# Kernel optimization log

Measured on AMD Instinct MI355X. Metric: run time of the kernel, lower is better.

Reference implementation:

```python
import jax, jax.numpy as jnp
import numpy as np

DIM = 2048
DIM_SEQ = 2048
HEADS = 4
BATCH = 4
LN_EPS = 1e-5  # torch nn.LayerNorm default


def setup_inputs() -> dict:
    key = jax.random.key(0)
    k1, k2 = jax.random.split(key)
    init_eps = 0.001 / DIM_SEQ
    x = jax.random.normal(k1, (BATCH, DIM_SEQ, DIM), dtype=jnp.float32)
    weight = jax.random.uniform(k2, (HEADS, DIM_SEQ, DIM_SEQ), dtype=jnp.float32,
                                minval=-init_eps, maxval=init_eps)
    bias = jnp.ones((HEADS, DIM_SEQ), dtype=jnp.float32)
    ln_gamma = jnp.ones((DIM // 2,), dtype=jnp.float32)
    ln_beta = jnp.zeros((DIM // 2,), dtype=jnp.float32)
    return {"x": x, "weight": weight, "bias": bias,
            "ln_gamma": ln_gamma, "ln_beta": ln_beta}


def _layernorm(x, gamma, beta):
    mu = jnp.mean(x, axis=-1, keepdims=True)
    var = jnp.mean(jnp.square(x - mu), axis=-1, keepdims=True)
    return (x - mu) * jax.lax.rsqrt(var + LN_EPS) * gamma + beta


def reference(x, weight, bias, ln_gamma, ln_beta):
    b, n, _ = x.shape
    h = HEADS
    res, gate = jnp.split(x, 2, axis=-1)          # each [b, n, dim/2]
    gate = _layernorm(gate, ln_gamma, ln_beta)
    w = weight[:, :n, :n]                          # [h, n, n]
    bi = bias[:, :n]                               # [h, n]
    # causal: zero strictly-upper triangle (output pos m attends n <= m)
    w = w * jnp.tril(jnp.ones((n, n), dtype=w.dtype))
    d = gate.shape[-1] // h
    gate = gate.reshape(b, n, h, d).transpose(0, 2, 1, 3)   # [b, h, n, d]
    gate = jnp.einsum('bhnd,hmn->bhmd', gate, w)
    gate = gate + bi[None, :, :, None]
    gate = gate.transpose(0, 2, 1, 3).reshape(b, n, h * d)  # [b, n, dim/2]
    return gate * res
```

## Files before the change

kernel.cpp:

```cpp
#include <hip/hip_runtime.h>
#include <hip/hip_bf16.h>

constexpr int Bb = 4;
constexpr int Nn = 2048;
constexpr int DX = 2048;
constexpr int GD = 1024;
constexpr int DH = 256;
constexpr int BM = 128, BD = 128, BK = 32;

typedef short short8v __attribute__((ext_vector_type(8)));
typedef short short4v __attribute__((ext_vector_type(4)));
typedef float f32x4   __attribute__((ext_vector_type(4)));

static __device__ __forceinline__ short f2bf(float f) {
    return __builtin_bit_cast(short, __float2bfloat16(f));
}

__global__ __launch_bounds__(256) void ln_stats_kernel(const float* __restrict__ x,
                                                       float2* __restrict__ mr) {
    int t = threadIdx.x;
    int row = blockIdx.x * 4 + (t >> 6);
    int lane = t & 63;
    const float4* xr = reinterpret_cast<const float4*>(x + (size_t)row * DX + GD);
    float s = 0.f, ss = 0.f;
#pragma unroll
    for (int q = 0; q < 4; ++q) {
        float4 v = xr[q * 64 + lane];
        s  += v.x + v.y + v.z + v.w;
        ss += v.x*v.x + v.y*v.y + v.z*v.z + v.w*v.w;
    }
#pragma unroll
    for (int off = 32; off >= 1; off >>= 1) {
        s  += __shfl_down(s,  off, 64);
        ss += __shfl_down(ss, off, 64);
    }
    if (lane == 0) {
        float m   = s * (1.f / GD);
        float var = ss * (1.f / GD) - m * m;
        mr[row] = make_float2(m, rsqrtf(var + 1e-5f));
    }
}

__global__ __launch_bounds__(256, 3) void sgu_mfma_kernel(
    const float* __restrict__ x, const float* __restrict__ w,
    const float* __restrict__ bias, const float* __restrict__ gamma,
    const float* __restrict__ beta, const float2* __restrict__ mr,
    float* __restrict__ out)
{
    __shared__ __align__(16) short Ws[2][BM * BK];
    __shared__ __align__(16) short Gs[2][BD * BK];
    __shared__ __align__(16) float2 MR[Nn];

    const int t  = threadIdx.x;
    const int bx = blockIdx.x;
    const int dc = bx & 1;
    const int h  = (bx >> 1) & 3;
    const int b  = bx >> 3;
    const int y  = blockIdx.y;
    const int mt = (y < 8) ? (15 - 2 * y) : ((y - 8) * 2);
    const int m0 = mt * BM;
    const int cb = h * DH + dc * BD;
    const int nk = 4 * mt + 4;

    const int lane = t & 63;
    const int wv = t >> 6;
    const int wm = wv >> 1, wc = wv & 1;
    const int g  = lane >> 4;
    const int lr = lane & 15;

    const int sw_row = t >> 1;
    const int sw_kh  = t & 1;
    const int sg_c4  = (t & 31) * 4;
    const int sg_k4  = (t >> 5) * 4;

    const float* xb   = x + (size_t)b * Nn * DX;
    const float* wrow = w + ((size_t)h * Nn + m0 + sw_row) * Nn + sw_kh * 16;
    const float* gsrc = xb + GD + cb + sg_c4;
    const float2* mrb = mr + b * Nn;

    float4 gmv = *reinterpret_cast<const float4*>(gamma + cb + sg_c4);
    float4 btv = *reinterpret_cast<const float4*>(beta  + cb + sg_c4);
    const float gmc[4] = {gmv.x, gmv.y, gmv.z, gmv.w};
    const float btc[4] = {btv.x, btv.y, btv.z, btv.w};

    f32x4 acc[4][4] = {};
    float4 wreg[4];
    float4 greg[4];

    auto LOADT = [&](int kt) {
        const int n0 = kt * BK;
#pragma unroll
        for (int q = 0; q < 4; ++q)
            wreg[q] = *reinterpret_cast<const float4*>(wrow + n0 + q * 4);
#pragma unroll
        for (int j = 0; j < 4; ++j)
            greg[j] = *reinterpret_cast<const float4*>(gsrc + (size_t)(n0 + sg_k4 + j) * DX);
    };

    auto STAGE = [&](int buf, int kt) {
        const int n0 = kt * BK;
        const int m = m0 + sw_row;
        short8v wlo, whi;
#pragma unroll
        for (int q = 0; q < 4; ++q) {
            float vv[4] = {wreg[q].x, wreg[q].y, wreg[q].z, wreg[q].w};
#pragma unroll
            for (int e = 0; e < 4; ++e) {
                int i = q * 4 + e;
                int n = n0 + sw_kh * 16 + i;
                short bfv = f2bf((n <= m) ? vv[e] : 0.f);
                if (i < 8) wlo[i] = bfv; else whi[i - 8] = bfv;
            }
        }
        char* wl = (char*)&Ws[buf][0];
        unsigned wb = (unsigned)(sw_row * 64 + sw_kh * 32);
        unsigned sz = ((unsigned)(sw_row >> 1) & 3u) << 4;
        *reinterpret_cast<short8v*>(wl + ((wb)      ^ sz)) = wlo;
        *reinterpret_cast<short8v*>(wl + ((wb + 16) ^ sz)) = whi;
        float muk[4], rsk[4];
        {
            f32x4 p0 = *reinterpret_cast<const f32x4*>(&MR[n0 + sg_k4]);
            f32x4 p1 = *reinterpret_cast<const f32x4*>(&MR[n0 + sg_k4 + 2]);
            muk[0] = p0[0]; rsk[0] = p0[1]; muk[1] = p0[2]; rsk[1] = p0[3];
            muk[2] = p1[0]; rsk[2] = p1[1]; muk[3] = p1[2]; rsk[3] = p1[3];
        }
        float gv[4][4];
        gv[0][0]=greg[0].x; gv[0][1]=greg[0].y; gv[0][2]=greg[0].z; gv[0][3]=greg[0].w;
        gv[1][0]=greg[1].x; gv[1][1]=greg[1].y; gv[1][2]=greg[1].z; gv[1][3]=greg[1].w;
        gv[2][0]=greg[2].x; gv[2][1]=greg[2].y; gv[2][2]=greg[2].z; gv[2][3]=greg[2].w;
        gv[3][0]=greg[3].x; gv[3][1]=greg[3].y; gv[3][2]=greg[3].z; gv[3][3]=greg[3].w;
        char* glp = (char*)&Gs[buf][0];
#pragma unroll
        for (int cc = 0; cc < 4; ++cc) {
            short4v pk;
#pragma unroll
            for (int j = 0; j < 4; ++j)
                pk[j] = f2bf((gv[j][cc] - muk[j]) * rsk[j] * gmc[cc] + btc[cc]);
            int c = sg_c4 + cc;
            unsigned off = (unsigned)(c * 64 + sg_k4 * 2);
            off ^= ((unsigned)(c >> 1) & 3u) << 4;
            *reinterpret_cast<short4v*>(glp + off) = pk;
        }
    };

    auto COMPUTE = [&](int buf) {
        const char* wl  = (const char*)&Ws[buf][0];
        const char* glp = (const char*)&Gs[buf][0];
        short8v af[4], bfr[4];
#pragma unroll
        for (int fi = 0; fi < 4; ++fi) {
            int row = wm * 64 + fi * 16 + lr;
            unsigned off = (unsigned)(row * 64 + g * 16);
            off ^= ((unsigned)(row >> 1) & 3u) << 4;
            af[fi] = *reinterpret_cast<const short8v*>(wl + off);
        }
#pragma unroll
        for (int fj = 0; fj < 4; ++fj) {
            int c = wc * 64 + fj * 16 + lr;
            unsigned off = (unsigned)(c * 64 + g * 16);
            off ^= ((unsigned)(c >> 1) & 3u) << 4;
            bfr[fj] = *reinterpret_cast<const short8v*>(glp + off);
        }
#pragma unroll
        for (int fi = 0; fi < 4; ++fi)
#pragma unroll
            for (int fj = 0; fj < 4; ++fj)
                acc[fi][fj] = __builtin_amdgcn_mfma_f32_16x16x32_bf16(
                    af[fi], bfr[fj], acc[fi][fj], 0, 0, 0);
    };

    const int nstage = nk * BK;
    for (int i = t; i < nstage; i += 256)
        MR[i] = mrb[i];
    LOADT(0);
    __syncthreads();
    STAGE(0, 0);
    __syncthreads();

    int cur = 0;
    for (int kt = 0; kt < nk; ++kt) {
        const bool more = (kt + 1 < nk);
        if (more) LOADT(kt + 1);
        COMPUTE(cur);
        if (more) STAGE(cur ^ 1, kt + 1);
        __syncthreads();
        cur ^= 1;
    }

#pragma unroll
    for (int fi = 0; fi < 4; ++fi) {
#pragma unroll
        for (int r = 0; r < 4; ++r) {
            int m = m0 + wm * 64 + fi * 16 + g * 4 + r;
            float bv = bias[h * Nn + m];
            const float* resrow = xb + (size_t)m * DX + cb;
            float* orow = out + ((size_t)b * Nn + m) * GD + cb;
#pragma unroll
            for (int fj = 0; fj < 4; ++fj) {
                int c = wc * 64 + fj * 16 + lr;
                orow[c] = (acc[fi][fj][r] + bv) * resrow[c];
            }
        }
    }
}

extern "C" void kernel_launch(void* const* d_in, const int* in_sizes, int n_in,
                              void* d_out, int out_size, void* d_ws, size_t ws_size,
                              hipStream_t stream) {
    const float* x     = (const float*)d_in[0];
    const float* w     = (const float*)d_in[1];
    const float* bias  = (const float*)d_in[2];
    const float* gamma = (const float*)d_in[3];
    const float* beta  = (const float*)d_in[4];
    float* out  = (float*)d_out;
    float2* mrw = (float2*)d_ws;

    ln_stats_kernel<<<Bb * Nn / 4, 256, 0, stream>>>(x, mrw);

    dim3 grid(32, 16, 1);
    sgu_mfma_kernel<<<grid, 256, 0, stream>>>(x, w, bias, gamma, beta, mrw, out);
}
```

Baseline: 253.2 us.

## Pre-convert weights and normalized gate to swizzled bf16 tiles, stage via direct LDS loads

Adds two pre-pass kernels. One converts the causal-masked weight to bf16 and the other applies layernorm to the gate and converts it to bf16. Both write tiles already in the swizzled LDS layout into workspace. The main GEMM kernel then fills shared memory with global_load_lds 16-byte copies instead of loading fp32 into registers and converting in the loop. This halves the bytes the main loop reads, moves conversion and normalization out of it, and frees registers. The cost is extra launches and an extra write and read of the bf16 copies, and the kernel returns without doing anything if the workspace is too small.

```diff
diff --git a/kernel.cpp b/kernel.cpp
--- a/kernel.cpp
+++ b/kernel.cpp
@@ -1,19 +1,24 @@
 #include <hip/hip_runtime.h>
 #include <hip/hip_bf16.h>
+
 
 constexpr int Bb = 4;
 constexpr int Nn = 2048;
 constexpr int DX = 2048;
 constexpr int GD = 1024;
 constexpr int DH = 256;
-constexpr int BM = 128, BD = 128, BK = 32;
 
 typedef short short8v __attribute__((ext_vector_type(8)));
-typedef short short4v __attribute__((ext_vector_type(4)));
 typedef float f32x4   __attribute__((ext_vector_type(4)));
 
 static __device__ __forceinline__ short f2bf(float f) {
     return __builtin_bit_cast(short, __float2bfloat16(f));
+}
+
+static __device__ __forceinline__ void gll16(const void* g, void* l) {
+    __builtin_amdgcn_global_load_lds(
+        (const __attribute__((address_space(1))) void*)g,
+        (__attribute__((address_space(3))) void*)l, 16, 0, 0);
 }
 
 __global__ __launch_bounds__(256) void ln_stats_kernel(const float* __restrict__ x,
@@ -41,15 +46,80 @@
     }
 }
 
+__global__ __launch_bounds__(256) void wcvt_kernel(const float* __restrict__ w,
+                                                   short* __restrict__ wt) {
+    const int hm = blockIdx.x;
+    const int kt = blockIdx.y;
+    const int mt = hm & 15, h = hm >> 4;
+    if (kt > 4 * mt + 3) return;
+    const int t = threadIdx.x;
+    const int m0 = mt * 128, n0 = kt * 32;
+    short* tile = wt + ((size_t)hm * 64 + kt) * 4096;
+#pragma unroll
+    for (int j = 0; j < 2; ++j) {
+        int s  = 2 * t + j;
+        int r  = s >> 2;
+        int k8 = (s & 3) ^ ((r >> 1) & 3);
+        const float* src = w + (size_t)(h * Nn + m0 + r) * Nn + n0 + k8 * 8;
+        float4 a = *reinterpret_cast<const float4*>(src);
+        float4 c = *reinterpret_cast<const float4*>(src + 4);
+        const int m = m0 + r, nb0 = n0 + k8 * 8;
+        float av[8] = {a.x, a.y, a.z, a.w, c.x, c.y, c.z, c.w};
+        short8v o;
+#pragma unroll
+        for (int e = 0; e < 8; ++e) o[e] = f2bf((nb0 + e) <= m ? av[e] : 0.f);
+        *reinterpret_cast<short8v*>(tile + s * 8) = o;
+    }
+}
+
+__global__ __launch_bounds__(256) void gcvt_kernel(const float* __restrict__ x,
+                                                   const float* __restrict__ gamma,
+                                                   const float* __restrict__ beta,
+                                                   const float2* __restrict__ mr,
+                                                   short* __restrict__ gt) {
+    __shared__ short T[128 * 136];
+    const int nb = blockIdx.x, cblk = blockIdx.y, b = blockIdx.z;
+    const int t = threadIdx.x;
+    const int n0b = nb * 128, c0 = cblk * 128;
+    const int c4 = (t & 31) * 4, rg = t >> 5;
+
+    const float* src = x + (size_t)b * Nn * DX + GD + c0 + c4;
+    float4 gm = *reinterpret_cast<const float4*>(gamma + c0 + c4);
+    float4 bt = *reinterpret_cast<const float4*>(beta  + c0 + c4);
+    const float2* mrb = mr + b * Nn + n0b;
+
+#pragma unroll
+    for (int i = 0; i < 16; ++i) {
+        int n = i * 8 + rg;
+        float2 ms = mrb[n];
+        float4 v  = *reinterpret_cast<const float4*>(src + (size_t)(n0b + n) * DX);
+        T[(c4 + 0) * 136 + n] = f2bf((v.x - ms.x) * ms.y * gm.x + bt.x);
+        T[(c4 + 1) * 136 + n] = f2bf((v.y - ms.x) * ms.y * gm.y + bt.y);
+        T[(c4 + 2) * 136 + n] = f2bf((v.z - ms.x) * ms.y * gm.z + bt.z);
+        T[(c4 + 3) * 136 + n] = f2bf((v.w - ms.x) * ms.y * gm.w + bt.w);
+    }
+    __syncthreads();
+#pragma unroll
+    for (int kq = 0; kq < 4; ++kq) {
+        short* tile = gt + ((size_t)(b * 8 + cblk) * 64 + (nb * 4 + kq)) * 4096;
+#pragma unroll
+        for (int j = 0; j < 2; ++j) {
+            int s  = 2 * t + j;
+            int c  = s >> 2;
+            int n8 = (s & 3) ^ ((c >> 1) & 3);
+            short8v v = *reinterpret_cast<const short8v*>(&T[c * 136 + kq * 32 + n8 * 8]);
+            *reinterpret_cast<short8v*>(tile + s * 8) = v;
+        }
+    }
+}
+
 __global__ __launch_bounds__(256, 3) void sgu_mfma_kernel(
-    const float* __restrict__ x, const float* __restrict__ w,
-    const float* __restrict__ bias, const float* __restrict__ gamma,
-    const float* __restrict__ beta, const float2* __restrict__ mr,
+    const float* __restrict__ x, const short* __restrict__ wt,
+    const short* __restrict__ gt, const float* __restrict__ bias,
     float* __restrict__ out)
 {
-    __shared__ __align__(16) short Ws[2][BM * BK];
-    __shared__ __align__(16) short Gs[2][BD * BK];
-    __shared__ __align__(16) float2 MR[Nn];
+    __shared__ __align__(16) short WS[2][4096];
+    __shared__ __align__(16) short GS[2][4096];
 
     const int t  = threadIdx.x;
     const int bx = blockIdx.x;
@@ -58,8 +128,8 @@
     const int b  = bx >> 3;
     const int y  = blockIdx.y;
     const int mt = (y < 8) ? (15 - 2 * y) : ((y - 8) * 2);
-    const int m0 = mt * BM;
-    const int cb = h * DH + dc * BD;
+    const int m0 = mt * 128;
+    const int cb = h * DH + dc * 128;
     const int nk = 4 * mt + 4;
 
     const int lane = t & 63;
@@ -68,85 +138,27 @@
     const int g  = lane >> 4;
     const int lr = lane & 15;
 
-    const int sw_row = t >> 1;
-    const int sw_kh  = t & 1;
-    const int sg_c4  = (t & 31) * 4;
-    const int sg_k4  = (t >> 5) * 4;
-
-    const float* xb   = x + (size_t)b * Nn * DX;
-    const float* wrow = w + ((size_t)h * Nn + m0 + sw_row) * Nn + sw_kh * 16;
-    const float* gsrc = xb + GD + cb + sg_c4;
-    const float2* mrb = mr + b * Nn;
-
-    float4 gmv = *reinterpret_cast<const float4*>(gamma + cb + sg_c4);
-    float4 btv = *reinterpret_cast<const float4*>(beta  + cb + sg_c4);
-    const float gmc[4] = {gmv.x, gmv.y, gmv.z, gmv.w};
-    const float btc[4] = {btv.x, btv.y, btv.z, btv.w};
+    const char* wtb = (const char*)wt + ((size_t)(h * 16 + mt) * 64) * 8192;
+    const char* gtb = (const char*)gt + ((size_t)(b * 8 + h * 2 + dc) * 64) * 8192;
+    const int soff = wv * 2048 + lane * 16;
 
     f32x4 acc[4][4] = {};
-    float4 wreg[4];
-    float4 greg[4];
-
-    auto LOADT = [&](int kt) {
-        const int n0 = kt * BK;
-#pragma unroll
-        for (int q = 0; q < 4; ++q)
-            wreg[q] = *reinterpret_cast<const float4*>(wrow + n0 + q * 4);
-#pragma unroll
-        for (int j = 0; j < 4; ++j)
-            greg[j] = *reinterpret_cast<const float4*>(gsrc + (size_t)(n0 + sg_k4 + j) * DX);
+
+    auto STAGE = [&](int buf, int kt) {
+        const char* ws = wtb + (size_t)kt * 8192 + soff;
+        const char* gs = gtb + (size_t)kt * 8192 + soff;
+        short* wd = &WS[buf][wv * 1024];
+        short* gd = &GS[buf][wv * 1024];
+        gll16(ws,        wd);
+        gll16(ws + 1024, wd + 512);
+        gll16(gs,        gd);
+        gll16(gs + 1024, gd + 512);
     };
 
-    auto STAGE = [&](int buf, int kt) {
-        const int n0 = kt * BK;
-        const int m = m0 + sw_row;
-        short8v wlo, whi;
-#pragma unroll
-        for (int q = 0; q < 4; ++q) {
-            float vv[4] = {wreg[q].x, wreg[q].y, wreg[q].z, wreg[q].w};
-#pragma unroll
-            for (int e = 0; e < 4; ++e) {
-                int i = q * 4 + e;
-                int n = n0 + sw_kh * 16 + i;
-                short bfv = f2bf((n <= m) ? vv[e] : 0.f);
-                if (i < 8) wlo[i] = bfv; else whi[i - 8] = bfv;
-            }
-        }
-        char* wl = (char*)&Ws[buf][0];
-        unsigned wb = (unsigned)(sw_row * 64 + sw_kh * 32);
-        unsigned sz = ((unsigned)(sw_row >> 1) & 3u) << 4;
-        *reinterpret_cast<short8v*>(wl + ((wb)      ^ sz)) = wlo;
-        *reinterpret_cast<short8v*>(wl + ((wb + 16) ^ sz)) = whi;
-        float muk[4], rsk[4];
-        {
-            f32x4 p0 = *reinterpret_cast<const f32x4*>(&MR[n0 + sg_k4]);
-            f32x4 p1 = *reinterpret_cast<const f32x4*>(&MR[n0 + sg_k4 + 2]);
-            muk[0] = p0[0]; rsk[0] = p0[1]; muk[1] = p0[2]; rsk[1] = p0[3];
-            muk[2] = p1[0]; rsk[2] = p1[1]; muk[3] = p1[2]; rsk[3] = p1[3];
-        }
-        float gv[4][4];
-        gv[0][0]=greg[0].x; gv[0][1]=greg[0].y; gv[0][2]=greg[0].z; gv[0][3]=greg[0].w;
-        gv[1][0]=greg[1].x; gv[1][1]=greg[1].y; gv[1][2]=greg[1].z; gv[1][3]=greg[1].w;
-        gv[2][0]=greg[2].x; gv[2][1]=greg[2].y; gv[2][2]=greg[2].z; gv[2][3]=greg[2].w;
-        gv[3][0]=greg[3].x; gv[3][1]=greg[3].y; gv[3][2]=greg[3].z; gv[3][3]=greg[3].w;
-        char* glp = (char*)&Gs[buf][0];
-#pragma unroll
-        for (int cc = 0; cc < 4; ++cc) {
-            short4v pk;
-#pragma unroll
-            for (int j = 0; j < 4; ++j)
-                pk[j] = f2bf((gv[j][cc] - muk[j]) * rsk[j] * gmc[cc] + btc[cc]);
-            int c = sg_c4 + cc;
-            unsigned off = (unsigned)(c * 64 + sg_k4 * 2);
-            off ^= ((unsigned)(c >> 1) & 3u) << 4;
-            *reinterpret_cast<short4v*>(glp + off) = pk;
-        }
-    };
-
     auto COMPUTE = [&](int buf) {
-        const char* wl  = (const char*)&Ws[buf][0];
-        const char* glp = (const char*)&Gs[buf][0];
-        short8v af[4], bfr[4];
+        const char* wl = (const char*)&WS[buf][0];
+        const char* gl = (const char*)&GS[buf][0];
+        short8v af[4], bf[4];
 #pragma unroll
         for (int fi = 0; fi < 4; ++fi) {
             int row = wm * 64 + fi * 16 + lr;
@@ -159,34 +171,27 @@
             int c = wc * 64 + fj * 16 + lr;
             unsigned off = (unsigned)(c * 64 + g * 16);
             off ^= ((unsigned)(c >> 1) & 3u) << 4;
-            bfr[fj] = *reinterpret_cast<const short8v*>(glp + off);
+            bf[fj] = *reinterpret_cast<const short8v*>(gl + off);
         }
 #pragma unroll
         for (int fi = 0; fi < 4; ++fi)
 #pragma unroll
             for (int fj = 0; fj < 4; ++fj)
                 acc[fi][fj] = __builtin_amdgcn_mfma_f32_16x16x32_bf16(
-                    af[fi], bfr[fj], acc[fi][fj], 0, 0, 0);
+                    af[fi], bf[fj], acc[fi][fj], 0, 0, 0);
     };
 
-    const int nstage = nk * BK;
-    for (int i = t; i < nstage; i += 256)
-        MR[i] = mrb[i];
-    LOADT(0);
-    __syncthreads();
     STAGE(0, 0);
     __syncthreads();
-
     int cur = 0;
     for (int kt = 0; kt < nk; ++kt) {
-        const bool more = (kt + 1 < nk);
-        if (more) LOADT(kt + 1);
+        if (kt + 1 < nk) STAGE(cur ^ 1, kt + 1);
         COMPUTE(cur);
-        if (more) STAGE(cur ^ 1, kt + 1);
         __syncthreads();
         cur ^= 1;
     }
 
+    const float* xb = x + (size_t)b * Nn * DX;
 #pragma unroll
     for (int fi = 0; fi < 4; ++fi) {
 #pragma unroll
@@ -212,11 +217,19 @@
     const float* bias  = (const float*)d_in[2];
     const float* gamma = (const float*)d_in[3];
     const float* beta  = (const float*)d_in[4];
-    float* out  = (float*)d_out;
+    float* out = (float*)d_out;
+
+    const size_t MR_BYTES = 64 * 1024;
+    const size_t GT_BYTES = (size_t)16 * 1024 * 1024;
+    const size_t WT_BYTES = (size_t)32 * 1024 * 1024;
+    if (ws_size < MR_BYTES + GT_BYTES + WT_BYTES) return;
+
     float2* mrw = (float2*)d_ws;
+    short*  gtw = (short*)((char*)d_ws + MR_BYTES);
+    short*  wtw = (short*)((char*)d_ws + MR_BYTES + GT_BYTES);
 
     ln_stats_kernel<<<Bb * Nn / 4, 256, 0, stream>>>(x, mrw);
-
-    dim3 grid(32, 16, 1);
-    sgu_mfma_kernel<<<grid, 256, 0, stream>>>(x, w, bias, gamma, beta, mrw, out);
-}
+    gcvt_kernel<<<dim3(16, 8, Bb), 256, 0, stream>>>(x, gamma, beta, mrw, gtw);
+    wcvt_kernel<<<dim3(64, 64), 256, 0, stream>>>(w, wtw);
+    sgu_mfma_kernel<<<dim3(32, 16), 256, 0, stream>>>(x, wtw, gtw, bias, out);
+}
```

New measurement: 217.6 us. 1.16x faster.
